# Optimization experiments

Hardware: AMD Instinct MI355X
Metric: run time of the kernel (lower is better)

Reference implementation:

```python
import jax, jax.numpy as jnp
import numpy as np

L, S, N, E, H = 1024, 1024, 8, 1024, 16

def setup_inputs() -> dict:
    key = jax.random.key(0)
    k0, k1, k2, k3 = jax.random.split(key, 4)
    query = jax.random.normal(k0, (L, N, E), jnp.float32)
    key_t = jax.random.normal(k1, (S, N, E), jnp.float32)
    in_proj_weight = jax.random.normal(k2, (3 * E, E), jnp.float32) * (1.0 / np.sqrt(E))
    in_proj_bias = jnp.zeros((3 * E,), jnp.float32)
    attn_bias = jax.random.normal(k3, (N * H, L, S), jnp.float32) * 0.02
    return {"query": query, "key": key_t, "in_proj_weight": in_proj_weight,
            "in_proj_bias": in_proj_bias, "attn_bias": attn_bias}

def reference(query, key, in_proj_weight, in_proj_bias, attn_bias):
    tgt_len, bsz, embed_dim = query.shape
    head_dim = embed_dim // H
    scaling = float(head_dim) ** -0.5  # scale_factor = 1
    # q/k projections: first two embed_dim-row slices of in_proj_weight
    q = query @ in_proj_weight[:embed_dim].T + in_proj_bias[:embed_dim]
    k = key @ in_proj_weight[embed_dim:2 * embed_dim].T + in_proj_bias[embed_dim:2 * embed_dim]
    q = q * scaling
    # (L, N, E) -> (N*H, L, hd)
    q = q.reshape(tgt_len, bsz * H, head_dim).transpose(1, 0, 2)
    k = k.reshape(-1, bsz * H, head_dim).transpose(1, 0, 2)
    # scores: (N*H, L, S), additive bias, then stable softmax
    scores = jnp.einsum('bld,bsd->bls', q, k) + attn_bias
    attn_output_weights = jax.nn.softmax(scores, axis=-1)
    return attn_output_weights
```

## Files before the change

kernel.cpp:

```cpp
#include <hip/hip_runtime.h>
#include <hip/hip_bf16.h>
#include <stdint.h>

#define L_DIM 1024
#define S_DIM 1024
#define N_DIM 8
#define E_DIM 1024
#define H_DIM 16
#define HD    64
#define BH    (N_DIM*H_DIM)
#define M_ROWS (L_DIM*N_DIM)

#define AS1 __attribute__((address_space(1)))
#define AS3 __attribute__((address_space(3)))

typedef __bf16 bf16x8 __attribute__((ext_vector_type(8)));
typedef float  f32x4  __attribute__((ext_vector_type(4)));
typedef _Float16 f16;
typedef _Float16 f16x8 __attribute__((ext_vector_type(8)));
typedef unsigned short u16;
typedef unsigned short u16x8 __attribute__((ext_vector_type(8)));

__device__ inline u16 f2bf(float x){
  unsigned int u = __float_as_uint(x);
  u = (u + 0x7FFFu + ((u >> 16) & 1u)) >> 16;
  return (u16)u;
}

__global__ __launch_bounds__(256) void convert_kernel(
    const float* __restrict__ query, const float* __restrict__ key,
    const float* __restrict__ w,
    u16* __restrict__ qbf, u16* __restrict__ kbf,
    u16* __restrict__ wq, u16* __restrict__ wk)
{
  const int QN = M_ROWS*E_DIM;
  const int WN = E_DIM*E_DIM;
  const int total8 = (2*QN + 2*WN)/8;
  int stride = gridDim.x*blockDim.x;
  for (int g = blockIdx.x*blockDim.x + threadIdx.x; g < total8; g += stride) {
    int base = g*8;
    const float* src; u16* dst; float scale = 1.0f;
    if (base < QN)           { src = query + base;      dst = qbf + base; }
    else if (base < 2*QN)    { src = key + (base-QN);   dst = kbf + (base-QN); }
    else if (base < 2*QN+WN) { src = w + (base-2*QN);   dst = wq + (base-2*QN); scale = 0.125f; }
    else                     { src = w + (base-2*QN);   dst = wk + (base-2*QN-WN); }
    float4 v0 = *(const float4*)(src);
    float4 v1 = *(const float4*)(src+4);
    u16x8 o;
    o[0]=f2bf(v0.x*scale); o[1]=f2bf(v0.y*scale); o[2]=f2bf(v0.z*scale); o[3]=f2bf(v0.w*scale);
    o[4]=f2bf(v1.x*scale); o[5]=f2bf(v1.y*scale); o[6]=f2bf(v1.z*scale); o[7]=f2bf(v1.w*scale);
    *(u16x8*)dst = o;
  }
}

__global__ __launch_bounds__(256) void proj_gemm(
    const u16* __restrict__ A, const u16* __restrict__ W,
    const float* __restrict__ bias, float bscale,
    u16* __restrict__ C)
{
  __shared__ __align__(16) u16 As[128*32];
  __shared__ __align__(16) u16 Bs[128*32];
  const int t = threadIdx.x;
  const int lane = t & 63;
  const int w = t >> 6;
  const int wr = w >> 1, wc = w & 1;
  const int rowTile = blockIdx.x * 128;
  const int colTile = blockIdx.y * 128;

  f32x4 acc[4][4];
  #pragma unroll
  for (int m=0;m<4;m++)
    #pragma unroll
    for (int n=0;n<4;n++) acc[m][n] = (f32x4){0.f,0.f,0.f,0.f};

  uint32_t asBase = (uint32_t)(uintptr_t)&As[0];
  uint32_t bsBase = (uint32_t)(uintptr_t)&Bs[0];
  const char* Ab = (const char*)A;
  const char* Wb = (const char*)W;

  for (int kt = 0; kt < 32; ++kt) {
    __syncthreads();
    #pragma unroll
    for (int issue = 0; issue < 2; ++issue) {
      int o = issue*4096 + t*16;
      int row  = o >> 6;
      int colb = o & 63;
      const char* ga = Ab + (size_t)(rowTile + row)*2048 + kt*64 + colb;
      const char* gb = Wb + (size_t)(colTile + row)*2048 + kt*64 + colb;
      uint32_t la = asBase + issue*4096 + (w<<10);
      uint32_t lb = bsBase + issue*4096 + (w<<10);
      __builtin_amdgcn_global_load_lds(
          (const AS1 void*)(uintptr_t)ga, (AS3 void*)(uintptr_t)la, 16, 0, 0);
      __builtin_amdgcn_global_load_lds(
          (const AS1 void*)(uintptr_t)gb, (AS3 void*)(uintptr_t)lb, 16, 0, 0);
    }
    __syncthreads();

    bf16x8 af[4], bfr[4];
    int krow = (lane >> 4) * 16;
    #pragma unroll
    for (int m=0;m<4;m++) {
      int r = wr*64 + m*16 + (lane&15);
      af[m] = *(const bf16x8*)((const char*)As + r*64 + krow);
    }
    #pragma unroll
    for (int n=0;n<4;n++) {
      int r = wc*64 + n*16 + (lane&15);
      bfr[n] = *(const bf16x8*)((const char*)Bs + r*64 + krow);
    }
    #pragma unroll
    for (int m=0;m<4;m++)
      #pragma unroll
      for (int n=0;n<4;n++)
        acc[m][n] = __builtin_amdgcn_mfma_f32_16x16x32_bf16(af[m], bfr[n], acc[m][n], 0,0,0);
  }

  #pragma unroll
  for (int n2=0;n2<4;n2++) {
    int gcol = colTile + wc*64 + n2*16 + (lane&15);
    int h = gcol >> 6, d = gcol & 63;
    float bv = bias[gcol]*bscale;
    #pragma unroll
    for (int m=0;m<4;m++) {
      int grow0 = rowTile + wr*64 + m*16 + ((lane>>4)<<2);
      #pragma unroll
      for (int r=0;r<4;r++) {
        int grow = grow0 + r;
        int l = grow >> 3, nn = grow & 7;
        C[((size_t)(nn*16 + h)*1024 + l)*64 + d] = f2bf(acc[m][n2][r] + bv);
      }
    }
  }
}

__global__ __launch_bounds__(256) void attn_softmax(
    const u16* __restrict__ Qh, const u16* __restrict__ Kh,
    const float* __restrict__ bias, float* __restrict__ out)
{
  __shared__ __align__(16) char scb[16*2048];
  __shared__ __align__(16) char kbuf[8192];
  const int t = threadIdx.x;
  const int lane = t & 63;
  const int w = t >> 6;
  const int ltile = blockIdx.x;
  const int b = blockIdx.y;

  const float* bias_base = bias + (((size_t)b<<10) + (size_t)ltile*16)*1024;
  f32x4 breg[4][4];
  #pragma unroll
  for (int rr=0;rr<4;rr++) {
    const float* brow = bias_base + (size_t)(rr*4 + w)*1024 + lane*8;
    #pragma unroll
    for (int p=0;p<4;p++)
      breg[rr][p] = *(const f32x4*)(brow + (p>>1)*512 + (p&1)*4);
  }
  __builtin_amdgcn_sched_barrier(0);

  const char* Kb = (const char*)(Kh + (size_t)b*1024*64);
  const u16*  Qb = Qh + (size_t)b*1024*64 + (size_t)ltile*16*64;

  int qoff = (lane&15)*64 + (lane>>4)*8;
  bf16x8 a0 = *(const bf16x8*)(Qb + qoff);
  bf16x8 a1 = *(const bf16x8*)(Qb + qoff + 32);

  const int rowBase = (lane>>4)*4;
  uint32_t kbase = (uint32_t)(uintptr_t)&kbuf[0];

  for (int g = 0; g < 16; ++g) {
    __syncthreads();
    #pragma unroll
    for (int rd = 0; rd < 2; ++rd) {
      int o = rd*4096 + t*16;
      int src = o ^ (((o>>7)&7)<<4);
      __builtin_amdgcn_global_load_lds(
          (const AS1 void*)(uintptr_t)(Kb + (size_t)g*8192 + src),
          (AS3 void*)(uintptr_t)(kbase + rd*4096 + (w<<10)), 16, 0, 0);
    }
    __syncthreads();

    int r = w*16 + (lane&15);
    int byte0 = r*128 + ((lane>>4)*16);
    int swzk = (r&7)<<4;
    bf16x8 b0 = *(const bf16x8*)(kbuf + ((byte0      ) ^ swzk));
    bf16x8 b1 = *(const bf16x8*)(kbuf + ((byte0 + 64 ) ^ swzk));
    f32x4 acc = {0.f,0.f,0.f,0.f};
    acc = __builtin_amdgcn_mfma_f32_16x16x32_bf16(a0, b0, acc, 0,0,0);
    acc = __builtin_amdgcn_mfma_f32_16x16x32_bf16(a1, b1, acc, 0,0,0);

    int scol = g*64 + w*16 + (lane & 15);
    #pragma unroll
    for (int rr=0;rr<4;rr++) {
      int row = rowBase + rr;
      int byte = (row*2048 + scol*2) ^ ((row&7)<<4);
      *(f16*)(scb + byte) = (f16)acc[rr];
    }
  }
  __syncthreads();

  #pragma unroll
  for (int rr=0;rr<4;rr++) {
    int row = rr*4 + w;
    int l_glob = ltile*16 + row;
    float* orow = out + ((size_t)b*1024 + l_glob)*1024;
    const int rswz = (row&7)<<4;
    float v[16];
    float mx = -1e30f;
    #pragma unroll
    for (int it=0; it<2; ++it) {
      int cb = it*1024 + lane*16;
      f16x8 s8 = *(const f16x8*)(scb + ((row*2048 + cb) ^ rswz));
      #pragma unroll
      for (int j=0;j<4;j++) v[it*8+j]   = (float)s8[j]   + breg[rr][it*2][j];
      #pragma unroll
      for (int j=0;j<4;j++) v[it*8+4+j] = (float)s8[4+j] + breg[rr][it*2+1][j];
    }
    #pragma unroll
    for (int j=0;j<16;j++) mx = fmaxf(mx, v[j]);
    #pragma unroll
    for (int off=32; off>0; off>>=1) mx = fmaxf(mx, __shfl_xor(mx, off, 64));
    float sum = 0.f;
    #pragma unroll
    for (int j=0;j<16;j++) { v[j] = __expf(v[j]-mx); sum += v[j]; }
    #pragma unroll
    for (int off=32; off>0; off>>=1) sum += __shfl_xor(sum, off, 64);
    float inv = 1.0f / sum;
    #pragma unroll
    for (int it=0; it<2; ++it) {
      int col = it*512 + lane*8;
      f32x4 o4a = { v[it*8+0]*inv, v[it*8+1]*inv, v[it*8+2]*inv, v[it*8+3]*inv };
      f32x4 o4b = { v[it*8+4]*inv, v[it*8+5]*inv, v[it*8+6]*inv, v[it*8+7]*inv };
      *(f32x4*)(orow + col)     = o4a;
      *(f32x4*)(orow + col + 4) = o4b;
    }
  }
}

extern "C" void kernel_launch(void* const* d_in, const int* in_sizes, int n_in,
                              void* d_out, int out_size, void* d_ws, size_t ws_size,
                              hipStream_t stream) {
  const float* query = (const float*)d_in[0];
  const float* key   = (const float*)d_in[1];
  const float* w     = (const float*)d_in[2];
  const float* bias  = (const float*)d_in[3];
  const float* abias = (const float*)d_in[4];
  float* out = (float*)d_out;

  char* ws = (char*)d_ws;
  const size_t QKB = (size_t)M_ROWS*E_DIM*2;
  const size_t WB  = (size_t)E_DIM*E_DIM*2;
  u16* qbf = (u16*)ws;  ws += QKB;
  u16* kbf = (u16*)ws;  ws += QKB;
  u16* wq  = (u16*)ws;  ws += WB;
  u16* wk  = (u16*)ws;  ws += WB;
  u16* Qh  = (u16*)ws;  ws += QKB;
  u16* Kh  = (u16*)ws;  ws += QKB;

  hipLaunchKernelGGL(convert_kernel, dim3(2048), dim3(256), 0, stream,
                     query, key, w, qbf, kbf, wq, wk);
  hipLaunchKernelGGL(proj_gemm, dim3(64, 8), dim3(256), 0, stream,
                     qbf, wq, bias, 0.125f, Qh);
  hipLaunchKernelGGL(proj_gemm, dim3(64, 8), dim3(256), 0, stream,
                     kbf, wk, bias + 1024, 1.0f, Kh);
  hipLaunchKernelGGL(attn_softmax, dim3(64, 128), dim3(256), 0, stream,
                     Qh, Kh, abias, out);
}
```

Before: 348.7 us.

## Double-buffer per-wave K staging and fold bias into MFMA accumulator

K tiles now go into per-wave double-buffered LDS slices. The next chunk is prefetched while the current one is consumed, with s_waitcnt vmcnt in place of two block-wide __syncthreads per iteration. The additive bias is loaded per chunk in MFMA output layout and used as the accumulator's initial value, which removes the large upfront bias register preload. The trade-offs are that bias is now read as scalar, less coalesced loads, and the scores stored in f16 now include the bias, which slightly changes rounding.

```diff
diff --git a/kernel.cpp b/kernel.cpp
--- a/kernel.cpp
+++ b/kernel.cpp
@@ -138,63 +138,76 @@
     const float* __restrict__ bias, float* __restrict__ out)
 {
   __shared__ __align__(16) char scb[16*2048];
-  __shared__ __align__(16) char kbuf[8192];
+  __shared__ __align__(16) char kbuf[2][4][2048];
   const int t = threadIdx.x;
   const int lane = t & 63;
   const int w = t >> 6;
   const int ltile = blockIdx.x;
   const int b = blockIdx.y;
-
-  const float* bias_base = bias + (((size_t)b<<10) + (size_t)ltile*16)*1024;
-  f32x4 breg[4][4];
-  #pragma unroll
-  for (int rr=0;rr<4;rr++) {
-    const float* brow = bias_base + (size_t)(rr*4 + w)*1024 + lane*8;
-    #pragma unroll
-    for (int p=0;p<4;p++)
-      breg[rr][p] = *(const f32x4*)(brow + (p>>1)*512 + (p&1)*4);
-  }
-  __builtin_amdgcn_sched_barrier(0);
-
-  const char* Kb = (const char*)(Kh + (size_t)b*1024*64);
-  const u16*  Qb = Qh + (size_t)b*1024*64 + (size_t)ltile*16*64;
-
-  int qoff = (lane&15)*64 + (lane>>4)*8;
-  bf16x8 a0 = *(const bf16x8*)(Qb + qoff);
-  bf16x8 a1 = *(const bf16x8*)(Qb + qoff + 32);
-
-  const int rowBase = (lane>>4)*4;
-  uint32_t kbase = (uint32_t)(uintptr_t)&kbuf[0];
-
+  const int q16 = lane & 15;
+  const int sg  = lane >> 4;
+
+  const char* Kb = (const char*)(Kh + (size_t)b*65536);
+  const u16*  Qb = Qh + (size_t)b*65536 + (size_t)ltile*1024;
+
+  bf16x8 a0 = *(const bf16x8*)(Qb + q16*64 + sg*8);
+  bf16x8 a1 = *(const bf16x8*)(Qb + q16*64 + sg*8 + 32);
+
+  const int stg_row = lane >> 3;
+  const int stg_off = (((lane & 7) ^ stg_row) << 4);
+  const char* Kst = Kb + w*2048 + stg_row*128 + stg_off;
+  const uint32_t kw0 = (uint32_t)(uintptr_t)&kbuf[0][w][0];
+  const uint32_t kw1 = (uint32_t)(uintptr_t)&kbuf[1][w][0];
+
+  const float* bl = bias + ((size_t)b*1024 + ltile*16 + sg*4)*1024 + w*16 + q16;
+
+  float bv[2][4];
+
+  #define ISSUE_CHUNK(gg, dd) do {                                          \
+    const char* s_ = Kst + (gg)*8192;                                       \
+    uint32_t d_ = (dd) ? kw1 : kw0;                                         \
+    __builtin_amdgcn_global_load_lds(                                       \
+        (const AS1 void*)(uintptr_t)s_, (AS3 void*)(uintptr_t)d_, 16, 0, 0);\
+    __builtin_amdgcn_global_load_lds(                                       \
+        (const AS1 void*)(uintptr_t)(s_+1024),                              \
+        (AS3 void*)(uintptr_t)(d_+1024), 16, 0, 0);                         \
+    bv[dd][0] = bl[(gg)*64];                                                \
+    bv[dd][1] = bl[(gg)*64 + 1024];                                         \
+    bv[dd][2] = bl[(gg)*64 + 2048];                                         \
+    bv[dd][3] = bl[(gg)*64 + 3072];                                         \
+  } while(0)
+
+  ISSUE_CHUNK(0, 0);
+
+  const int c0 = ((sg     ^ (q16 & 7)) << 4);
+  const int c1 = (((4+sg) ^ (q16 & 7)) << 4);
+
+  #pragma unroll
   for (int g = 0; g < 16; ++g) {
-    __syncthreads();
-    #pragma unroll
-    for (int rd = 0; rd < 2; ++rd) {
-      int o = rd*4096 + t*16;
-      int src = o ^ (((o>>7)&7)<<4);
-      __builtin_amdgcn_global_load_lds(
-          (const AS1 void*)(uintptr_t)(Kb + (size_t)g*8192 + src),
-          (AS3 void*)(uintptr_t)(kbase + rd*4096 + (w<<10)), 16, 0, 0);
-    }
-    __syncthreads();
-
-    int r = w*16 + (lane&15);
-    int byte0 = r*128 + ((lane>>4)*16);
-    int swzk = (r&7)<<4;
-    bf16x8 b0 = *(const bf16x8*)(kbuf + ((byte0      ) ^ swzk));
-    bf16x8 b1 = *(const bf16x8*)(kbuf + ((byte0 + 64 ) ^ swzk));
-    f32x4 acc = {0.f,0.f,0.f,0.f};
+    const int d = g & 1;
+    if (g < 15) ISSUE_CHUNK(g+1, d^1);
+    if (g < 15) { asm volatile("s_waitcnt vmcnt(6)" ::: "memory"); }
+    else        { asm volatile("s_waitcnt vmcnt(0)" ::: "memory"); }
+    __builtin_amdgcn_sched_barrier(0);
+
+    const char* kw = (const char*)&kbuf[d][w][0];
+    bf16x8 b0 = *(const bf16x8*)(kw + q16*128 + c0);
+    bf16x8 b1 = *(const bf16x8*)(kw + q16*128 + c1);
+    f32x4 acc = { bv[d][0], bv[d][1], bv[d][2], bv[d][3] };
     acc = __builtin_amdgcn_mfma_f32_16x16x32_bf16(a0, b0, acc, 0,0,0);
     acc = __builtin_amdgcn_mfma_f32_16x16x32_bf16(a1, b1, acc, 0,0,0);
 
-    int scol = g*64 + w*16 + (lane & 15);
-    #pragma unroll
-    for (int rr=0;rr<4;rr++) {
-      int row = rowBase + rr;
+    const int scol = g*64 + w*16 + q16;
+    #pragma unroll
+    for (int rr=0; rr<4; ++rr) {
+      int row = sg*4 + rr;
       int byte = (row*2048 + scol*2) ^ ((row&7)<<4);
       *(f16*)(scb + byte) = (f16)acc[rr];
     }
-  }
+    __builtin_amdgcn_sched_barrier(0);
+  }
+  #undef ISSUE_CHUNK
+
   __syncthreads();
 
   #pragma unroll
@@ -210,9 +223,7 @@
       int cb = it*1024 + lane*16;
       f16x8 s8 = *(const f16x8*)(scb + ((row*2048 + cb) ^ rswz));
       #pragma unroll
-      for (int j=0;j<4;j++) v[it*8+j]   = (float)s8[j]   + breg[rr][it*2][j];
-      #pragma unroll
-      for (int j=0;j<4;j++) v[it*8+4+j] = (float)s8[4+j] + breg[rr][it*2+1][j];
+      for (int j=0;j<8;j++) v[it*8+j] = (float)s8[j];
     }
     #pragma unroll
     for (int j=0;j<16;j++) mx = fmaxf(mx, v[j]);
```

Result: no change. 345.5 us (median of 3 runs) (-0.9%).
